# Kernel tuning notes

Measured on AMD Instinct MI355X. Metric: run time of the kernel, lower is better.

The kernel has to match this reference:

```python
import jax, jax.numpy as jnp
import numpy as np

HID = 1024      # hidden_size (embedding dim, GRU input)
RNN = 1024      # rnn_hidden_size
VOCAB = 50000   # max_node
STEPS = 1024    # num_steps
SOS = 0


def setup_inputs() -> dict:
    key = jax.random.key(0)
    ks = jax.random.split(key, 8)
    s = 0.02
    return {
        "inputs": jax.random.randint(ks[0], (STEPS,), 0, VOCAB),
        "z": jax.random.normal(ks[1], (RNN,), jnp.float32),
        "emb_W": jax.random.uniform(ks[2], (VOCAB, HID), jnp.float32, -0.001, 0.001),
        "out_b": jnp.full((VOCAB,), 0.01, jnp.float32),
        "h2e_W": jax.random.normal(ks[3], (HID, RNN), jnp.float32) * s,
        "h2e_b": jnp.full((HID,), 0.01, jnp.float32),
        "W_ih": jax.random.normal(ks[4], (3 * RNN, HID), jnp.float32) * s,
        "W_hh": jax.random.normal(ks[5], (3 * RNN, RNN), jnp.float32) * s,
        "b_ih": jnp.zeros((3 * RNN,), jnp.float32),
        "b_hh": jnp.zeros((3 * RNN,), jnp.float32),
    }


def reference(inputs, z, emb_W, out_b, h2e_W, h2e_b, W_ih, W_hh, b_ih, b_hh):
    R = RNN

    def gru_cell(h, x):
        gi = W_ih @ x + b_ih          # (3R,)
        gh = W_hh @ h + b_hh          # (3R,)
        r = jax.nn.sigmoid(gi[:R] + gh[:R])
        zg = jax.nn.sigmoid(gi[R:2 * R] + gh[R:2 * R])
        n = jnp.tanh(gi[2 * R:] + r * gh[2 * R:])
        return (1.0 - zg) * n + zg * h

    # teacher forcing: step i consumes token_{i-1} (SOS for i=1), target is inputs[i]
    step_tokens = jnp.concatenate([jnp.array([SOS], dtype=inputs.dtype), inputs[1:-1]])
    targets = inputs[1:]

    def step(h, tok_tgt):
        tok, tgt = tok_tgt
        x = emb_W[tok]                              # embedding lookup (HID,)
        h_new = gru_cell(h, x)                      # (RNN,)
        e = h2e_W @ h_new + h2e_b                   # (HID,)
        logp = jax.nn.log_softmax(emb_W @ e + out_b)  # tied weights, (VOCAB,)
        return h_new, (-logp[tgt], jnp.argmax(logp))

    _, (losses, preds) = jax.lax.scan(step, z, (step_tokens, targets))
    loss = jnp.sum(losses)
    outputs = jnp.zeros((1, inputs.shape[0]), dtype=jnp.int32).at[0, 1:].set(preds.astype(jnp.int32))
    return loss, outputs
```

## Files before the change

### kernel.cpp

```cpp
#include <hip/hip_runtime.h>
#include <math.h>

#define NV      50000
#define T_STEPS 1023
#define KDIM    1024
#define NCH     391
#define TAU     4e-5f
typedef unsigned long long ull;


__global__ __launch_bounds__(256) void k_gather(const int* __restrict__ inputs,
                                                const float* __restrict__ emb,
                                                float* __restrict__ X) {
  const int t = blockIdx.x;
  const int tid = threadIdx.x;
  float4 v = make_float4(0.f, 0.f, 0.f, 0.f);
  if (t < T_STEPS) {
    const int tok = (t == 0) ? 0 : inputs[t];
    v = *(const float4*)&emb[(size_t)tok * KDIM + tid * 4];
  }
  *(float4*)&X[(size_t)t * KDIM + tid * 4] = v;
}

__global__ __launch_bounds__(256) void k_gemm_ffd(const float* __restrict__ A,
                                                  const float* __restrict__ B,
                                                  const float* __restrict__ bias,
                                                  double* __restrict__ C,
                                                  int N, int K) {
  __shared__ float As[32][68];
  __shared__ float Bs[32][68];
  const int tid = threadIdx.x;
  const int bx = blockIdx.x, by = blockIdx.y;
  const int lr = tid >> 2;
  const int lk = (tid & 3) * 8;
  const float* Ap = A + (size_t)(by * 64 + lr) * K + lk;
  const float* Bp = B + (size_t)(bx * 64 + lr) * K + lk;
  const int r0 = (tid >> 4) * 4;
  const int c0 = (tid & 15) * 4;
  double acc[4][4] = {};
  for (int kc = 0; kc < K; kc += 32) {
    const float4 a0 = *(const float4*)(Ap + kc);
    const float4 a1 = *(const float4*)(Ap + kc + 4);
    const float4 b0 = *(const float4*)(Bp + kc);
    const float4 b1 = *(const float4*)(Bp + kc + 4);
    __syncthreads();
    As[lk+0][lr]=a0.x; As[lk+1][lr]=a0.y; As[lk+2][lr]=a0.z; As[lk+3][lr]=a0.w;
    As[lk+4][lr]=a1.x; As[lk+5][lr]=a1.y; As[lk+6][lr]=a1.z; As[lk+7][lr]=a1.w;
    Bs[lk+0][lr]=b0.x; Bs[lk+1][lr]=b0.y; Bs[lk+2][lr]=b0.z; Bs[lk+3][lr]=b0.w;
    Bs[lk+4][lr]=b1.x; Bs[lk+5][lr]=b1.y; Bs[lk+6][lr]=b1.z; Bs[lk+7][lr]=b1.w;
    __syncthreads();
#pragma unroll
    for (int kk = 0; kk < 32; ++kk) {
      const float4 av = *(const float4*)&As[kk][r0];
      const float4 bv = *(const float4*)&Bs[kk][c0];
      const double aa[4] = {av.x, av.y, av.z, av.w};
      const double bb[4] = {bv.x, bv.y, bv.z, bv.w};
#pragma unroll
      for (int i = 0; i < 4; ++i)
#pragma unroll
        for (int j = 0; j < 4; ++j)
          acc[i][j] = fma(aa[i], bb[j], acc[i][j]);
    }
  }
  const int row = by * 64 + r0;
  const int col = bx * 64 + c0;
#pragma unroll
  for (int i = 0; i < 4; ++i)
#pragma unroll
    for (int j = 0; j < 4; ++j)
      C[(size_t)(row + i) * N + col + j] = acc[i][j] + (double)bias[col + j];
}

__global__ __launch_bounds__(256) void k_gemm_dfd(const double* __restrict__ A,
                                                  const float* __restrict__ B,
                                                  const float* __restrict__ bias,
                                                  double* __restrict__ C,
                                                  float* __restrict__ Cf,
                                                  int N, int K) {
  __shared__ double As[32][68];
  __shared__ float  Bs[32][68];
  const int tid = threadIdx.x;
  const int bx = blockIdx.x, by = blockIdx.y;
  const int lr = tid >> 2;
  const int lk = (tid & 3) * 8;
  const double* Ap = A + (size_t)(by * 64 + lr) * K + lk;
  const float*  Bp = B + (size_t)(bx * 64 + lr) * K + lk;
  const int r0 = (tid >> 4) * 4;
  const int c0 = (tid & 15) * 4;
  double acc[4][4] = {};
  for (int kc = 0; kc < K; kc += 32) {
    double ar[8];
#pragma unroll
    for (int q = 0; q < 8; ++q) ar[q] = Ap[kc + q];
    const float4 b0 = *(const float4*)(Bp + kc);
    const float4 b1 = *(const float4*)(Bp + kc + 4);
    __syncthreads();
#pragma unroll
    for (int q = 0; q < 8; ++q) As[lk + q][lr] = ar[q];
    Bs[lk+0][lr]=b0.x; Bs[lk+1][lr]=b0.y; Bs[lk+2][lr]=b0.z; Bs[lk+3][lr]=b0.w;
    Bs[lk+4][lr]=b1.x; Bs[lk+5][lr]=b1.y; Bs[lk+6][lr]=b1.z; Bs[lk+7][lr]=b1.w;
    __syncthreads();
#pragma unroll
    for (int kk = 0; kk < 32; ++kk) {
      const double aa[4] = {As[kk][r0+0], As[kk][r0+1], As[kk][r0+2], As[kk][r0+3]};
      const float4 bv = *(const float4*)&Bs[kk][c0];
      const double bb[4] = {bv.x, bv.y, bv.z, bv.w};
#pragma unroll
      for (int i = 0; i < 4; ++i)
#pragma unroll
        for (int j = 0; j < 4; ++j)
          acc[i][j] = fma(aa[i], bb[j], acc[i][j]);
    }
  }
  const int row = by * 64 + r0;
  const int col = bx * 64 + c0;
#pragma unroll
  for (int i = 0; i < 4; ++i)
#pragma unroll
    for (int j = 0; j < 4; ++j) {
      const double o = acc[i][j] + (double)bias[col + j];
      C [(size_t)(row + i) * N + col + j] = o;
      Cf[(size_t)(row + i) * N + col + j] = (float)o;
    }
}

__global__ __launch_bounds__(512, 2) void k_recur(const float* __restrict__ z,
                                                  const float* __restrict__ Whh,
                                                  const float* __restrict__ bhh,
                                                  const double* __restrict__ GI,
                                                  double* H, ull* SA, ull* SB,
                                                  int* done) {
  __shared__ double hs[1024];
  const int tid = threadIdx.x;
  const int w = tid >> 6, l = tid & 63;
  const int ibase = blockIdx.x * 16 + w * 2;
  float wreg[6][16];
#pragma unroll
  for (int il = 0; il < 2; ++il)
#pragma unroll
    for (int g = 0; g < 3; ++g) {
      const float* wp = Whh + (size_t)(g * 1024 + ibase + il) * 1024 + l;
#pragma unroll
      for (int m = 0; m < 16; ++m) wreg[il * 3 + g][m] = wp[m * 64];
    }
  double bh[6];
#pragma unroll
  for (int il = 0; il < 2; ++il)
#pragma unroll
    for (int g = 0; g < 3; ++g) bh[il * 3 + g] = (double)bhh[g * 1024 + ibase + il];

  hs[tid]       = (double)z[tid];
  hs[tid + 512] = (double)z[tid + 512];
  double gi[6];
#pragma unroll
  for (int il = 0; il < 2; ++il)
#pragma unroll
    for (int g = 0; g < 3; ++g) gi[il * 3 + g] = GI[g * 1024 + ibase + il];
  __syncthreads();

  for (int t = 0; t < T_STEPS; ++t) {
    const bool more = (t + 1 < T_STEPS);
    const int p = t & 1;
    const bool gate = more && (t >= 2);
    int dv = 0x7FFFFFFF;
    if (gate && tid < 64)
      dv = __hip_atomic_load(done + p * 64 + tid,
                             __ATOMIC_RELAXED, __HIP_MEMORY_SCOPE_AGENT);
    double s[6] = {0.0, 0.0, 0.0, 0.0, 0.0, 0.0};
#pragma unroll
    for (int m = 0; m < 16; ++m) {
      const double hv = hs[l + 64 * m];
#pragma unroll
      for (int rr = 0; rr < 6; ++rr) s[rr] = fma((double)wreg[rr][m], hv, s[rr]);
    }
#pragma unroll
    for (int rr = 0; rr < 6; ++rr) {
      double v = s[rr];
#pragma unroll
      for (int mk = 32; mk >= 1; mk >>= 1) v += __shfl_xor(v, mk, 64);
      s[rr] = v;
    }
    double hn = 0.0;
    if (l < 2) {
      const int il = l;
      const double r  = 1.0 / (1.0 + exp(-(gi[il*3+0] + s[il*3+0] + bh[il*3+0])));
      const double zg = 1.0 / (1.0 + exp(-(gi[il*3+1] + s[il*3+1] + bh[il*3+1])));
      const double n  = tanh(gi[il*3+2] + r * (s[il*3+2] + bh[il*3+2]));
      hn = (1.0 - zg) * n + zg * hs[ibase + l];
    }
    double gin[6] = {0.0, 0.0, 0.0, 0.0, 0.0, 0.0};
    if (more) {
      const double* gp = GI + (size_t)(t + 1) * 3072;
#pragma unroll
      for (int il = 0; il < 2; ++il)
#pragma unroll
        for (int g = 0; g < 3; ++g) gin[il * 3 + g] = gp[g * 1024 + ibase + il];
    }
    if (gate && tid < 64) {
      while (!__all(dv >= t - 1)) {
        __builtin_amdgcn_s_sleep(1);
        dv = __hip_atomic_load(done + p * 64 + tid,
                               __ATOMIC_RELAXED, __HIP_MEMORY_SCOPE_AGENT);
      }
    }
    __syncthreads();
    if (l < 2) {
      const int gidx = ibase + l;
      __hip_atomic_store(H + (size_t)t * 1024 + gidx, hn,
                         __ATOMIC_RELAXED, __HIP_MEMORY_SCOPE_AGENT);
      if (more) {
        const ull hb  = (ull)__double_as_longlong(hn);
        const ull tag = ((ull)(t + 1)) << 32;
        __hip_atomic_store(SA + p * 1024 + gidx, tag | (hb >> 32),
                           __ATOMIC_RELAXED, __HIP_MEMORY_SCOPE_AGENT);
        __hip_atomic_store(SB + p * 1024 + gidx, tag | (hb & 0xFFFFFFFFull),
                           __ATOMIC_RELAXED, __HIP_MEMORY_SCOPE_AGENT);
      }
    }
    if (more) {
      const ull want = (ull)(t + 1);
      ull a0, b0, a1, b1;
      while (true) {
        a0 = __hip_atomic_load(SA + p * 1024 + tid,
                               __ATOMIC_RELAXED, __HIP_MEMORY_SCOPE_AGENT);
        b0 = __hip_atomic_load(SB + p * 1024 + tid,
                               __ATOMIC_RELAXED, __HIP_MEMORY_SCOPE_AGENT);
        if ((a0 >> 32) >= want && (b0 >> 32) >= want) break;
        __builtin_amdgcn_s_sleep(1);
      }
      while (true) {
        a1 = __hip_atomic_load(SA + p * 1024 + tid + 512,
                               __ATOMIC_RELAXED, __HIP_MEMORY_SCOPE_AGENT);
        b1 = __hip_atomic_load(SB + p * 1024 + tid + 512,
                               __ATOMIC_RELAXED, __HIP_MEMORY_SCOPE_AGENT);
        if ((a1 >> 32) >= want && (b1 >> 32) >= want) break;
        __builtin_amdgcn_s_sleep(1);
      }
      hs[tid]       = __longlong_as_double((long long)
                        (((a0 & 0xFFFFFFFFull) << 32) | (b0 & 0xFFFFFFFFull)));
      hs[tid + 512] = __longlong_as_double((long long)
                        (((a1 & 0xFFFFFFFFull) << 32) | (b1 & 0xFFFFFFFFull)));
      __syncthreads();
      if (tid == 0)
        __hip_atomic_store(done + p * 64 + blockIdx.x, t + 1,
                           __ATOMIC_RELAXED, __HIP_MEMORY_SCOPE_AGENT);
#pragma unroll
      for (int q = 0; q < 6; ++q) gi[q] = gin[q];
    }
  }
}

__global__ __launch_bounds__(256) void k_logits_f32(
    const float* __restrict__ Ef, const double* __restrict__ E64,
    const float* __restrict__ emb, const float* __restrict__ out_b,
    const int* __restrict__ inputs,
    float* __restrict__ candL, int* __restrict__ candI,
    float* __restrict__ Psum, float* __restrict__ Ttgt) {
  __shared__ float As[128][33];
  __shared__ float Bs[32][132];
  __shared__ int   WLs[2048];
  __shared__ int   WLv[2048];
  __shared__ float Lr[2048];
  __shared__ int   wcnt;
  const int tid = threadIdx.x;
  const int bx = blockIdx.x, by = blockIdx.y;
  const int arow = tid >> 1, akk = (tid & 1) * 16;
  const float* Ap = Ef + (size_t)(by * 128 + arow) * KDIM + akk;
  const int bcol = tid >> 1, bk = (tid & 1) * 16;
  const int brow = bx * 128 + bcol;
  const float* Bp = emb + (size_t)brow * KDIM + bk;
  const bool bvalid = brow < NV;
  const int r0 = (tid >> 4) * 8;
  const int c0 = (tid & 15) * 8;
  float acc[8][8] = {};
  for (int kc = 0; kc < KDIM; kc += 32) {
    float4 ar[4], br[4];
#pragma unroll
    for (int q = 0; q < 4; ++q) {
      ar[q] = *(const float4*)(Ap + kc + q * 4);
      br[q] = bvalid ? *(const float4*)(Bp + kc + q * 4)
                     : make_float4(0.f, 0.f, 0.f, 0.f);
    }
    __syncthreads();
#pragma unroll
    for (int q = 0; q < 4; ++q) {
      As[arow][akk + q*4 + 0] = ar[q].x;
      As[arow][akk + q*4 + 1] = ar[q].y;
      As[arow][akk + q*4 + 2] = ar[q].z;
      As[arow][akk + q*4 + 3] = ar[q].w;
      Bs[bk + q*4 + 0][bcol] = br[q].x;
      Bs[bk + q*4 + 1][bcol] = br[q].y;
      Bs[bk + q*4 + 2][bcol] = br[q].z;
      Bs[bk + q*4 + 3][bcol] = br[q].w;
    }
    __syncthreads();
#pragma unroll 4
    for (int kk = 0; kk < 32; ++kk) {
      float aa[8];
#pragma unroll
      for (int i = 0; i < 8; ++i) aa[i] = As[r0 + i][kk];
      const float4 bv0 = *(const float4*)&Bs[kk][c0];
      const float4 bv1 = *(const float4*)&Bs[kk][c0 + 4];
      const float bb[8] = {bv0.x, bv0.y, bv0.z, bv0.w,
                           bv1.x, bv1.y, bv1.z, bv1.w};
#pragma unroll
      for (int i = 0; i < 8; ++i)
#pragma unroll
        for (int j = 0; j < 8; ++j)
          acc[i][j] = fmaf(aa[i], bb[j], acc[i][j]);
    }
  }
  const int colb = bx * 128 + c0;
  float ob[8];
#pragma unroll
  for (int j = 0; j < 8; ++j) {
    const int v = colb + j;
    ob[j] = (v < NV) ? out_b[v] : 0.f;
  }
#pragma unroll
  for (int i = 0; i < 8; ++i) {
    const int s = by * 128 + r0 + i;
    const bool valid = (s < T_STEPS);
    if (tid == 0) wcnt = 0;
    __syncthreads();
    float af[8];
    float M = -3e38f;
#pragma unroll
    for (int j = 0; j < 8; ++j) {
      const int v = colb + j;
      af[j] = (v < NV) ? acc[i][j] + ob[j] : -3e38f;
      M = fmaxf(M, af[j]);
    }
#pragma unroll
    for (int mk = 1; mk <= 8; mk <<= 1) M = fmaxf(M, __shfl_xor(M, mk, 64));
    int myidx[8];
#pragma unroll
    for (int j = 0; j < 8; ++j) {
      const int v = colb + j;
      myidx[j] = -1;
      if (valid && v < NV && af[j] >= M - TAU) {
        const int ix = atomicAdd(&wcnt, 1);
        myidx[j] = ix;
        WLs[ix] = s;
        WLv[ix] = v;
      }
    }
    __syncthreads();
    const int nw = wcnt;
    for (int wi = tid; wi < nw; wi += 256) {
      const int ss = WLs[wi], vv = WLv[wi];
      const double* Er = E64 + (size_t)ss * KDIM;
      const float*  br2 = emb + (size_t)vv * KDIM;
      double d = 0.0;
#pragma unroll 4
      for (int k = 0; k < KDIM; ++k) d = fma(Er[k], (double)br2[k], d);
      Lr[wi] = (float)(d + (double)out_b[vv]);
    }
    __syncthreads();
    const int tgt = valid ? inputs[s + 1] : -1;
    float L1 = -3e38f, L2 = -3e38f;
    int   i1 = 0x7FFFFFFF, i2 = 0x7FFFFFFF;
    float se = 0.f, tv = -INFINITY;
#pragma unroll
    for (int j = 0; j < 8; ++j) {
      const int v = colb + j;
      if (v < NV) {
        se += expf(af[j] - 0.01f);
        if (v == tgt) tv = af[j];
        const float L = (myidx[j] >= 0) ? Lr[myidx[j]] : -3e38f;
        if (L > L1 || (L == L1 && v < i1)) { L2 = L1; i2 = i1; L1 = L; i1 = v; }
        else if (L > L2 || (L == L2 && v < i2)) { L2 = L; i2 = v; }
      }
    }
#pragma unroll
    for (int mk = 1; mk <= 8; mk <<= 1) {
      const float oL1 = __shfl_xor(L1, mk, 64); const int oi1 = __shfl_xor(i1, mk, 64);
      const float oL2 = __shfl_xor(L2, mk, 64); const int oi2 = __shfl_xor(i2, mk, 64);
      if (oL1 > L1 || (oL1 == L1 && oi1 < i1)) { L2 = L1; i2 = i1; L1 = oL1; i1 = oi1; }
      else if (oL1 > L2 || (oL1 == L2 && oi1 < i2)) { L2 = oL1; i2 = oi1; }
      if (oL2 > L1 || (oL2 == L1 && oi2 < i1)) { L2 = L1; i2 = i1; L1 = oL2; i1 = oi2; }
      else if (oL2 > L2 || (oL2 == L2 && oi2 < i2)) { L2 = oL2; i2 = oi2; }
      se += __shfl_xor(se, mk, 64);
      tv = fmaxf(tv, __shfl_xor(tv, mk, 64));
    }
    if (((tid & 15) == 0) && valid) {
      const size_t p = (size_t)s * (2 * NCH) + 2 * bx;
      candL[p] = L1;     candI[p] = i1;
      candL[p + 1] = L2; candI[p + 1] = i2;
      atomicAdd(&Psum[s], se);
      if (tv > -1e30f) Ttgt[s] = tv;
    }
    __syncthreads();
  }
}

__global__ __launch_bounds__(256) void k_preds(const float* __restrict__ candL,
                                               const int* __restrict__ candI,
                                               float* __restrict__ out) {
  __shared__ float sL[256];
  __shared__ int   sI[256];
  const int s = blockIdx.x;
  const int tid = threadIdx.x;
  const int n = 2 * NCH;
  const size_t base = (size_t)s * n;
  float m = -3e38f;
  for (int c = tid; c < n; c += 256) m = fmaxf(m, candL[base + c]);
  sL[tid] = m; __syncthreads();
  for (int st = 128; st > 0; st >>= 1) {
    if (tid < st) sL[tid] = fmaxf(sL[tid], sL[tid + st]);
    __syncthreads();
  }
  const float Lmax = sL[0];
  __syncthreads();
  float bq = -3e38f; int bi = 0x7FFFFFFF;
  for (int c = tid; c < n; c += 256) {
    const float L = candL[base + c];
    const int   v = candI[base + c];
    const float d = L - Lmax;
    const float q = d - 10.8125f;
    if (q > bq || (q == bq && v < bi)) { bq = q; bi = v; }
  }
  sL[tid] = bq; sI[tid] = bi; __syncthreads();
  for (int st = 128; st > 0; st >>= 1) {
    if (tid < st) {
      if (sL[tid + st] > sL[tid] ||
          (sL[tid + st] == sL[tid] && sI[tid + st] < sI[tid])) {
        sL[tid] = sL[tid + st]; sI[tid] = sI[tid + st];
      }
    }
    __syncthreads();
  }
  if (tid == 0) out[2 + s] = (float)sI[0];
}

__global__ __launch_bounds__(1024) void k_finish(const float* __restrict__ Psum,
                                                 const float* __restrict__ Ttgt,
                                                 float* __restrict__ out) {
  __shared__ double red[1024];
  const int s = threadIdx.x;
  double ls = 0.0;
  if (s < T_STEPS) ls = 0.01 + log((double)Psum[s]) - (double)Ttgt[s];
  red[s] = ls;
  __syncthreads();
  for (int st = 512; st > 0; st >>= 1) {
    if (s < st) red[s] += red[s + st];
    __syncthreads();
  }
  if (s == 0) out[0] = (float)red[0];
  if (s == 1) out[1] = 0.f;
}

extern "C" void kernel_launch(void* const* d_in, const int* in_sizes, int n_in,
                              void* d_out, int out_size, void* d_ws, size_t ws_size,
                              hipStream_t stream) {
  const int*   inputs = (const int*)  d_in[0];
  const float* z      = (const float*)d_in[1];
  const float* emb    = (const float*)d_in[2];
  const float* out_b  = (const float*)d_in[3];
  const float* h2eW   = (const float*)d_in[4];
  const float* h2eb   = (const float*)d_in[5];
  const float* Wih    = (const float*)d_in[6];
  const float* Whh    = (const float*)d_in[7];
  const float* bih    = (const float*)d_in[8];
  const float* bhh    = (const float*)d_in[9];

  char* ws8 = (char*)d_ws;
  ull*    SA    = (ull*)ws8;
  ull*    SB    = (ull*)(ws8 + 16384);
  int*    done  = (int*)(ws8 + 32768);
  float*  Psum  = (float*)(ws8 + 33280);
  float*  Ttgt  = (float*)(ws8 + 37376);
  float*  X     = (float*)(ws8 + 49152);
  char*   GIb   = ws8 + 49152 + (4u << 20);
  double* GI    = (double*)GIb;
  double* E     = GI;
  float*  candL = (float*)(GIb + (8u << 20));
  int*    candI = (int*)  (GIb + (8u << 20) + 3211264);
  float*  Ef    = (float*)(GIb + (8u << 20) + 6422528);
  double* H     = (double*)(GIb + (24u << 20));
  float*  out   = (float*)d_out;

  hipMemsetAsync(ws8, 0, 49152, stream);

  k_gather<<<1024, 256, 0, stream>>>(inputs, emb, X);
  k_gemm_ffd<<<dim3(48, 16), 256, 0, stream>>>(X, Wih, bih, GI, 3072, KDIM);
  k_recur<<<64, 512, 0, stream>>>(z, Whh, bhh, GI, H, SA, SB, done);
  k_gemm_dfd<<<dim3(16, 16), 256, 0, stream>>>(H, h2eW, h2eb, E, Ef, KDIM, KDIM);
  k_logits_f32<<<dim3(NCH, 8), 256, 0, stream>>>(Ef, E, emb, out_b, inputs,
                                                 candL, candI, Psum, Ttgt);
  k_preds<<<T_STEPS, 256, 0, stream>>>(candL, candI, out);
  k_finish<<<1, 1024, 0, stream>>>(Psum, Ttgt, out);
}
```

Measured before the change: 9.311 ms.

## Simplify recurrence sync with tagged-double exchange, fuse gather, shrink rescoring worklist

The recurrent kernel now publishes each hidden value as a single 64-bit word whose low two bits carry a step tag, replacing the split hi/lo tagged pairs and the separate per-block done-counter gate. This halves the global stores and polls per step and removes a gating barrier. The cost is that the two lowest mantissa bits of the shared state are overwritten. The embedding gather is fused into the input GEMM, dropping a kernel launch and the X buffer. The logits rescoring worklist is capped at a smaller shared size and uses a wave-cooperative dot product, with a serial per-thread path for overflow entries.

```diff
diff --git a/kernel.cpp b/kernel.cpp
--- a/kernel.cpp
+++ b/kernel.cpp
@@ -6,23 +6,12 @@
 #define KDIM    1024
 #define NCH     391
 #define TAU     4e-5f
+#define NWL     320
 typedef unsigned long long ull;
 
 
-__global__ __launch_bounds__(256) void k_gather(const int* __restrict__ inputs,
-                                                const float* __restrict__ emb,
-                                                float* __restrict__ X) {
-  const int t = blockIdx.x;
-  const int tid = threadIdx.x;
-  float4 v = make_float4(0.f, 0.f, 0.f, 0.f);
-  if (t < T_STEPS) {
-    const int tok = (t == 0) ? 0 : inputs[t];
-    v = *(const float4*)&emb[(size_t)tok * KDIM + tid * 4];
-  }
-  *(float4*)&X[(size_t)t * KDIM + tid * 4] = v;
-}
-
-__global__ __launch_bounds__(256) void k_gemm_ffd(const float* __restrict__ A,
+__global__ __launch_bounds__(256) void k_gemm_ffd(const int* __restrict__ inputs,
+                                                  const float* __restrict__ emb,
                                                   const float* __restrict__ B,
                                                   const float* __restrict__ bias,
                                                   double* __restrict__ C,
@@ -33,14 +22,17 @@
   const int bx = blockIdx.x, by = blockIdx.y;
   const int lr = tid >> 2;
   const int lk = (tid & 3) * 8;
-  const float* Ap = A + (size_t)(by * 64 + lr) * K + lk;
+  const int arow = by * 64 + lr;
+  const int tok = (arow == 0) ? 0 : ((arow < T_STEPS) ? inputs[arow] : -1);
+  const float* Ap = emb + (size_t)(tok < 0 ? 0 : tok) * K + lk;
   const float* Bp = B + (size_t)(bx * 64 + lr) * K + lk;
   const int r0 = (tid >> 4) * 4;
   const int c0 = (tid & 15) * 4;
   double acc[4][4] = {};
   for (int kc = 0; kc < K; kc += 32) {
-    const float4 a0 = *(const float4*)(Ap + kc);
-    const float4 a1 = *(const float4*)(Ap + kc + 4);
+    float4 a0 = make_float4(0.f, 0.f, 0.f, 0.f);
+    float4 a1 = make_float4(0.f, 0.f, 0.f, 0.f);
+    if (tok >= 0) { a0 = *(const float4*)(Ap + kc); a1 = *(const float4*)(Ap + kc + 4); }
     const float4 b0 = *(const float4*)(Bp + kc);
     const float4 b1 = *(const float4*)(Bp + kc + 4);
     __syncthreads();
@@ -128,8 +120,7 @@
                                                   const float* __restrict__ Whh,
                                                   const float* __restrict__ bhh,
                                                   const double* __restrict__ GI,
-                                                  double* H, ull* SA, ull* SB,
-                                                  int* done) {
+                                                  double* H, ull* ST) {
   __shared__ double hs[1024];
   const int tid = threadIdx.x;
   const int w = tid >> 6, l = tid & 63;
@@ -160,12 +151,6 @@
 
   for (int t = 0; t < T_STEPS; ++t) {
     const bool more = (t + 1 < T_STEPS);
-    const int p = t & 1;
-    const bool gate = more && (t >= 2);
-    int dv = 0x7FFFFFFF;
-    if (gate && tid < 64)
-      dv = __hip_atomic_load(done + p * 64 + tid,
-                             __ATOMIC_RELAXED, __HIP_MEMORY_SCOPE_AGENT);
     double s[6] = {0.0, 0.0, 0.0, 0.0, 0.0, 0.0};
 #pragma unroll
     for (int m = 0; m < 16; ++m) {
@@ -196,54 +181,31 @@
 #pragma unroll
         for (int g = 0; g < 3; ++g) gin[il * 3 + g] = gp[g * 1024 + ibase + il];
     }
-    if (gate && tid < 64) {
-      while (!__all(dv >= t - 1)) {
-        __builtin_amdgcn_s_sleep(1);
-        dv = __hip_atomic_load(done + p * 64 + tid,
-                               __ATOMIC_RELAXED, __HIP_MEMORY_SCOPE_AGENT);
-      }
-    }
-    __syncthreads();
+    __syncthreads();
+    const ull tg = (ull)((t + 1) & 3);
     if (l < 2) {
       const int gidx = ibase + l;
       __hip_atomic_store(H + (size_t)t * 1024 + gidx, hn,
                          __ATOMIC_RELAXED, __HIP_MEMORY_SCOPE_AGENT);
       if (more) {
-        const ull hb  = (ull)__double_as_longlong(hn);
-        const ull tag = ((ull)(t + 1)) << 32;
-        __hip_atomic_store(SA + p * 1024 + gidx, tag | (hb >> 32),
+        const ull hb = (ull)__double_as_longlong(hn);
+        __hip_atomic_store(ST + (size_t)((t + 1) & 1) * 1024 + gidx,
+                           (hb & ~3ull) | tg,
                            __ATOMIC_RELAXED, __HIP_MEMORY_SCOPE_AGENT);
-        __hip_atomic_store(SB + p * 1024 + gidx, tag | (hb & 0xFFFFFFFFull),
-                           __ATOMIC_RELAXED, __HIP_MEMORY_SCOPE_AGENT);
       }
     }
     if (more) {
-      const ull want = (ull)(t + 1);
-      ull a0, b0, a1, b1;
+      const ull* sp = ST + (size_t)((t + 1) & 1) * 1024 + 2 * tid;
+      ull w0, w1;
       while (true) {
-        a0 = __hip_atomic_load(SA + p * 1024 + tid,
-                               __ATOMIC_RELAXED, __HIP_MEMORY_SCOPE_AGENT);
-        b0 = __hip_atomic_load(SB + p * 1024 + tid,
-                               __ATOMIC_RELAXED, __HIP_MEMORY_SCOPE_AGENT);
-        if ((a0 >> 32) >= want && (b0 >> 32) >= want) break;
+        w0 = __hip_atomic_load(sp,     __ATOMIC_RELAXED, __HIP_MEMORY_SCOPE_AGENT);
+        w1 = __hip_atomic_load(sp + 1, __ATOMIC_RELAXED, __HIP_MEMORY_SCOPE_AGENT);
+        if ((w0 & 3ull) == tg && (w1 & 3ull) == tg) break;
         __builtin_amdgcn_s_sleep(1);
       }
-      while (true) {
-        a1 = __hip_atomic_load(SA + p * 1024 + tid + 512,
-                               __ATOMIC_RELAXED, __HIP_MEMORY_SCOPE_AGENT);
-        b1 = __hip_atomic_load(SB + p * 1024 + tid + 512,
-                               __ATOMIC_RELAXED, __HIP_MEMORY_SCOPE_AGENT);
-        if ((a1 >> 32) >= want && (b1 >> 32) >= want) break;
-        __builtin_amdgcn_s_sleep(1);
-      }
-      hs[tid]       = __longlong_as_double((long long)
-                        (((a0 & 0xFFFFFFFFull) << 32) | (b0 & 0xFFFFFFFFull)));
-      hs[tid + 512] = __longlong_as_double((long long)
-                        (((a1 & 0xFFFFFFFFull) << 32) | (b1 & 0xFFFFFFFFull)));
+      hs[2 * tid]     = __longlong_as_double((long long)w0);
+      hs[2 * tid + 1] = __longlong_as_double((long long)w1);
       __syncthreads();
-      if (tid == 0)
-        __hip_atomic_store(done + p * 64 + blockIdx.x, t + 1,
-                           __ATOMIC_RELAXED, __HIP_MEMORY_SCOPE_AGENT);
 #pragma unroll
       for (int q = 0; q < 6; ++q) gi[q] = gin[q];
     }
@@ -258,12 +220,13 @@
     float* __restrict__ Psum, float* __restrict__ Ttgt) {
   __shared__ float As[128][33];
   __shared__ float Bs[32][132];
-  __shared__ int   WLs[2048];
-  __shared__ int   WLv[2048];
-  __shared__ float Lr[2048];
+  __shared__ int   WLs[NWL];
+  __shared__ int   WLv[NWL];
+  __shared__ float Lr[NWL];
   __shared__ int   wcnt;
   const int tid = threadIdx.x;
   const int bx = blockIdx.x, by = blockIdx.y;
+  const int wave = tid >> 6, lane = tid & 63;
   const int arow = tid >> 1, akk = (tid & 1) * 16;
   const float* Ap = Ef + (size_t)(by * 128 + arow) * KDIM + akk;
   const int bcol = tid >> 1, bk = (tid & 1) * 16;
@@ -340,23 +303,37 @@
       myidx[j] = -1;
       if (valid && v < NV && af[j] >= M - TAU) {
         const int ix = atomicAdd(&wcnt, 1);
-        myidx[j] = ix;
-        WLs[ix] = s;
-        WLv[ix] = v;
-      }
-    }
-    __syncthreads();
-    const int nw = wcnt;
-    for (int wi = tid; wi < nw; wi += 256) {
+        if (ix < NWL) { myidx[j] = ix; WLs[ix] = s; WLv[ix] = v; }
+        else myidx[j] = -2;
+      }
+    }
+    __syncthreads();
+    const int nw = min(wcnt, NWL);
+    for (int wi = wave; wi < nw; wi += 4) {
       const int ss = WLs[wi], vv = WLv[wi];
       const double* Er = E64 + (size_t)ss * KDIM;
       const float*  br2 = emb + (size_t)vv * KDIM;
       double d = 0.0;
-#pragma unroll 4
-      for (int k = 0; k < KDIM; ++k) d = fma(Er[k], (double)br2[k], d);
-      Lr[wi] = (float)(d + (double)out_b[vv]);
-    }
-    __syncthreads();
+#pragma unroll
+      for (int m = 0; m < 16; ++m)
+        d = fma(Er[m * 64 + lane], (double)br2[m * 64 + lane], d);
+#pragma unroll
+      for (int mk = 32; mk >= 1; mk >>= 1) d += __shfl_xor(d, mk, 64);
+      if (lane == 0) Lr[wi] = (float)(d + (double)out_b[vv]);
+    }
+    __syncthreads();
+    float Lser[8];
+#pragma unroll
+    for (int j = 0; j < 8; ++j) {
+      Lser[j] = -3e38f;
+      if (myidx[j] == -2) {
+        const double* Er = E64 + (size_t)s * KDIM;
+        const float*  br2 = emb + (size_t)(colb + j) * KDIM;
+        double d = 0.0;
+        for (int k = 0; k < KDIM; ++k) d = fma(Er[k], (double)br2[k], d);
+        Lser[j] = (float)(d + (double)out_b[colb + j]);
+      }
+    }
     const int tgt = valid ? inputs[s + 1] : -1;
     float L1 = -3e38f, L2 = -3e38f;
     int   i1 = 0x7FFFFFFF, i2 = 0x7FFFFFFF;
@@ -367,7 +344,8 @@
       if (v < NV) {
         se += expf(af[j] - 0.01f);
         if (v == tgt) tv = af[j];
-        const float L = (myidx[j] >= 0) ? Lr[myidx[j]] : -3e38f;
+        const float L = (myidx[j] >= 0) ? Lr[myidx[j]]
+                      : ((myidx[j] == -2) ? Lser[j] : -3e38f);
         if (L > L1 || (L == L1 && v < i1)) { L2 = L1; i2 = i1; L1 = L; i1 = v; }
         else if (L > L2 || (L == L2 && v < i2)) { L2 = L; i2 = v; }
       }
@@ -465,13 +443,10 @@
   const float* bhh    = (const float*)d_in[9];
 
   char* ws8 = (char*)d_ws;
-  ull*    SA    = (ull*)ws8;
-  ull*    SB    = (ull*)(ws8 + 16384);
-  int*    done  = (int*)(ws8 + 32768);
-  float*  Psum  = (float*)(ws8 + 33280);
-  float*  Ttgt  = (float*)(ws8 + 37376);
-  float*  X     = (float*)(ws8 + 49152);
-  char*   GIb   = ws8 + 49152 + (4u << 20);
+  ull*    ST    = (ull*)ws8;
+  float*  Psum  = (float*)(ws8 + 16384);
+  float*  Ttgt  = (float*)(ws8 + 20480);
+  char*   GIb   = ws8 + 49152;
   double* GI    = (double*)GIb;
   double* E     = GI;
   float*  candL = (float*)(GIb + (8u << 20));
@@ -480,11 +455,11 @@
   double* H     = (double*)(GIb + (24u << 20));
   float*  out   = (float*)d_out;
 
-  hipMemsetAsync(ws8, 0, 49152, stream);
-
-  k_gather<<<1024, 256, 0, stream>>>(inputs, emb, X);
-  k_gemm_ffd<<<dim3(48, 16), 256, 0, stream>>>(X, Wih, bih, GI, 3072, KDIM);
-  k_recur<<<64, 512, 0, stream>>>(z, Whh, bhh, GI, H, SA, SB, done);
+  (void)hipMemsetAsync(ws8, 0, 24576, stream);
+
+  k_gemm_ffd<<<dim3(48, 16), 256, 0, stream>>>(inputs, emb, Wih, bih, GI,
+                                               3072, KDIM);
+  k_recur<<<64, 512, 0, stream>>>(z, Whh, bhh, GI, H, ST);
   k_gemm_dfd<<<dim3(16, 16), 256, 0, stream>>>(H, h2eW, h2eb, E, Ef, KDIM, KDIM);
   k_logits_f32<<<dim3(NCH, 8), 256, 0, stream>>>(Ef, E, emb, out_b, inputs,
                                                  candL, candI, Psum, Ttgt);
```

Result: slower. 9.643 ms (+3.6%).
